# Optimization experiments

Measured on AMD Instinct MI355X. Metric: run time of the kernel, lower is better.

Reference implementation:

```python
import jax, jax.numpy as jnp
import numpy as np

MUL0, MUL1, SCALARS_OUT = 16, 16, 128
L0, L1 = MUL0, MUL1 * 3            # 16, 48
PATH_NUMEL = MUL0 * MUL1 * SCALARS_OUT  # 32768 per path, two paths
EPS = 1e-5
# e3nn normalization: irrep_normalization='component' -> alpha = dim(ir_out) = 1;
# path_normalization='element' -> divide by sum over paths to same output of mul1*mul2 = 256+256 = 512.
PATH_COEFF = 1.0 / np.sqrt(512.0)
CG_110 = 1.0 / np.sqrt(3.0)  # wigner_3j(1,1,0)[i,j] = delta_ij/sqrt(3) (unit Frobenius norm)


def layer_norm(x, g, b):
    mu = jnp.mean(x, axis=-1, keepdims=True)
    var = jnp.mean(jnp.square(x - mu), axis=-1, keepdims=True)
    return (x - mu) * jax.lax.rsqrt(var + EPS) * g + b


def ff_block(x, g, b, w1, w2, b2):
    # LayerNorm -> Linear(no bias) -> SiLU -> Linear(bias); residual=False in both uses
    h = jax.nn.silu(layer_norm(x, g, b) @ w1)
    return h @ w2 + b2


def setup_inputs() -> dict:
    key = jax.random.key(0)
    ks = jax.random.split(key, 8)
    N = 2048
    return {
        "x": jax.random.normal(ks[0], (N, L0 + L1), dtype=jnp.float32),
        "we_ln_g": jnp.ones((L0,), jnp.float32),
        "we_ln_b": jnp.zeros((L0,), jnp.float32),
        "we_w1": jax.random.normal(ks[1], (L0, 4 * L0), jnp.float32) / np.sqrt(L0),
        "we_w2": jax.random.normal(ks[2], (4 * L0, 2 * PATH_NUMEL), jnp.float32) / np.sqrt(4 * L0),
        "we_b2": jnp.zeros((2 * PATH_NUMEL,), jnp.float32),
        "om_ln_g": jnp.ones((SCALARS_OUT,), jnp.float32),
        "om_ln_b": jnp.zeros((SCALARS_OUT,), jnp.float32),
        "om_w1": jax.random.normal(ks[3], (SCALARS_OUT, 4 * SCALARS_OUT), jnp.float32) / np.sqrt(SCALARS_OUT),
        "om_w2": jax.random.normal(ks[4], (4 * SCALARS_OUT, 1), jnp.float32) / np.sqrt(4 * SCALARS_OUT),
        "om_b2": jnp.zeros((1,), jnp.float32),
    }


def reference(x, we_ln_g, we_ln_b, we_w1, we_w2, we_b2,
              om_ln_g, om_ln_b, om_w1, om_w2, om_b2):
    N = x.shape[0]
    feats = x[:, :L0]                       # [N, 16] scalars (0e)
    x1 = x[:, L0:].reshape(N, MUL1, 3)      # [N, 16, 3] vectors (1o)

    # per-sample tensor-product weights (shared_weights=False)
    w = ff_block(feats, we_ln_g, we_ln_b, we_w1, we_w2, we_b2)  # [N, 65536]
    w0 = w[:, :PATH_NUMEL].reshape(N, MUL0, MUL0, SCALARS_OUT)
    w1 = w[:, PATH_NUMEL:].reshape(N, MUL1, MUL1, SCALARS_OUT)

    # path 0: 0e x 0e -> 0e  (uvw)
    o0 = jnp.einsum('nu,nv,nuvw->nw', feats, feats, w0)
    # path 1: 1o x 1o -> 0e  (uvw, CG = delta_ij/sqrt(3))
    o1 = jnp.einsum('nui,nvi,nuvw->nw', x1, x1, w1) * CG_110
    tp_out = PATH_COEFF * (o0 + o1)          # [N, 128]

    return ff_block(tp_out, om_ln_g, om_ln_b, om_w1, om_w2, om_b2)  # [N, 1]
```

## Files before the change

kernel.cpp:

```cpp
#include <hip/hip_runtime.h>
#include <hip/hip_bf16.h>
#include <cstdint>

#define EPS 1e-5f
#define PATH_COEFF 0.04419417382415922f
#define CG110     0.5773502691896258f

typedef __bf16 v8bf __attribute__((ext_vector_type(8)));
typedef float  v4f  __attribute__((ext_vector_type(4)));
typedef _Float16 v4h __attribute__((ext_vector_type(4)));

static __device__ __forceinline__ unsigned short f2bf(float x){
    unsigned int u = __builtin_bit_cast(unsigned int, x);
    u += 0x7fffu + ((u >> 16) & 1u);
    return (unsigned short)(u >> 16);
}
static __device__ __forceinline__ unsigned short f2h(float x){
    return __builtin_bit_cast(unsigned short, (_Float16)x);
}

__global__ __launch_bounds__(256)
void k_pre(const float* __restrict__ w2, const float* __restrict__ b2,
           unsigned short* __restrict__ Vt2,
           const float* __restrict__ om_w1, unsigned short* __restrict__ w1t,
           const float* __restrict__ x, const float* __restrict__ lng,
           const float* __restrict__ lnb, const float* __restrict__ we_w1,
           unsigned short* __restrict__ Q2, float* __restrict__ Ht, int N)
{
    __shared__ __align__(16) unsigned short tile[32][128];
    __shared__ __align__(16) uint4 qtile[64][4];
    __shared__ float htile[4][65];
    int b = blockIdx.x;
    int t = threadIdx.x;

    if (b < 260){
        int k    = b >> 2;
        int slab = b & 3;
        const float* srcbase = (k < 64) ? (w2 + (size_t)k * 65536) : b2;
        for (int chunk = 0; chunk < 4; ++chunk){
            int pbase = slab*128 + chunk*32;
            #pragma unroll
            for (int i = 0; i < 4; ++i){
                int g = t + 256*i;
                int ploc = g >> 5, c4 = g & 31;
                const float4 v = *(const float4*)(srcbase + (size_t)(pbase + ploc)*128 + c4*4);
                unsigned int w0 = (unsigned)f2bf(v.x) | ((unsigned)f2bf(v.y) << 16);
                unsigned int w1 = (unsigned)f2bf(v.z) | ((unsigned)f2bf(v.w) << 16);
                *(uint2*)&tile[ploc][c4*4] = make_uint2(w0, w1);
            }
            __syncthreads();
            int w = t & 127, h = t >> 7;
            int ps = slab*4 + chunk;
            unsigned int words[8];
            #pragma unroll
            for (int g2 = 0; g2 < 8; ++g2)
                words[g2] = (unsigned)tile[h*16 + g2*2][w] | ((unsigned)tile[h*16 + g2*2 + 1][w] << 16);
            unsigned short* dq0 = Vt2 + (((size_t)(k*16 + ps)*4 + 2*h    )*128 + w)*8;
            unsigned short* dq1 = Vt2 + (((size_t)(k*16 + ps)*4 + 2*h + 1)*128 + w)*8;
            *(uint4*)dq0 = make_uint4(words[0], words[1], words[2], words[3]);
            *(uint4*)dq1 = make_uint4(words[4], words[5], words[6], words[7]);
            __syncthreads();
        }
    } else if (b < 264){
        int j0 = (b - 260) * 128;
        for (int chunk = 0; chunk < 4; ++chunk){
            #pragma unroll
            for (int i = 0; i < 4; ++i){
                int g = t + 256*i;
                int wloc = g >> 5, c4 = g & 31;
                int w = chunk*32 + wloc;
                const float4 v = *(const float4*)(om_w1 + (size_t)w*512 + j0 + c4*4);
                unsigned int a = (unsigned)f2bf(v.x) | ((unsigned)f2bf(v.y) << 16);
                unsigned int bb = (unsigned)f2bf(v.z) | ((unsigned)f2bf(v.w) << 16);
                *(uint2*)&tile[wloc][c4*4] = make_uint2(a, bb);
            }
            __syncthreads();
            int jl = t & 127, h = t >> 7;
            unsigned int words[8];
            #pragma unroll
            for (int g2 = 0; g2 < 8; ++g2)
                words[g2] = (unsigned)tile[h*16 + g2*2][jl] | ((unsigned)tile[h*16 + g2*2 + 1][jl] << 16);
            unsigned short* dst = w1t + (size_t)(j0 + jl)*128 + chunk*32 + h*16;
            *(uint4*)dst       = make_uint4(words[0], words[1], words[2], words[3]);
            *(uint4*)(dst + 8) = make_uint4(words[4], words[5], words[6], words[7]);
            __syncthreads();
        }
    } else {
        int wv = t >> 6, lane = t & 63;
        int row0 = (b - 264)*4;
        int row  = row0 + wv;
        const float* xr = x + (size_t)row * 64;
        float f[16]; float mu = 0.f;
        #pragma unroll
        for (int u = 0; u < 16; ++u){ f[u] = xr[u]; mu += f[u]; }
        mu *= (1.f/16.f);
        float var = 0.f;
        #pragma unroll
        for (int u = 0; u < 16; ++u){ float d = f[u] - mu; var += d*d; }
        var *= (1.f/16.f);
        float inv = rsqrtf(var + EPS);
        float lnf[16];
        #pragma unroll
        for (int u = 0; u < 16; ++u) lnf[u] = (f[u]-mu)*inv*lng[u] + lnb[u];
        float h1 = 0.f;
        #pragma unroll
        for (int u = 0; u < 16; ++u) h1 += lnf[u] * we_w1[u*64 + lane];
        float h = h1 / (1.f + expf(-h1));
        htile[wv][lane] = h;
        if (lane == 0) htile[wv][64] = 1.f;

        union { unsigned short qs[8]; uint4 v; } qu;
        #pragma unroll
        for (int j = 0; j < 8; ++j){
            int p = lane*8 + j;
            float q;
            if (p < 256){
                int u = p >> 4, v = p & 15;
                q = PATH_COEFF * f[u] * f[v];
            } else {
                int pp = p - 256;
                int u = pp >> 4, v = pp & 15;
                const float* ya = xr + 16 + u*3;
                const float* yb = xr + 16 + v*3;
                q = (PATH_COEFF * CG110) * (ya[0]*yb[0] + ya[1]*yb[1] + ya[2]*yb[2]);
            }
            qu.qs[j] = f2bf(q);
        }
        qtile[lane][wv] = qu.v;
        __syncthreads();

        int rb = row0 >> 6, r64base = row0 & 63;
        {
            int slot = t >> 2, rr = t & 3;
            ((uint4*)Q2)[(size_t)rb*4096 + (size_t)slot*64 + r64base + rr] = qtile[slot][rr];
        }
        if (t < 65){
            float4 hv = make_float4(htile[0][t], htile[1][t], htile[2][t], htile[3][t]);
            *(float4*)(Ht + (size_t)t*N + row0) = hv;
        }
    }
}

__global__ __launch_bounds__(256, 2)
void k_main(const unsigned short* __restrict__ Q2, const unsigned short* __restrict__ Vt2,
            const float* __restrict__ Ht, unsigned short* __restrict__ partial, int N)
{
    __shared__ __align__(16) unsigned short stile[4][64*72];
    int g = blockIdx.x & 7;
    int j = blockIdx.x >> 3;
    int kg, mb;
    if (j < 64){ mb = j >> 2; kg = g*4 + (j & 3); }
    else { if (g != 0) return; mb = j - 64; kg = 32; }

    int tid  = threadIdx.x;
    int lane = tid & 63, wv = tid >> 6;
    int r2 = wv >> 1, c2 = wv & 1;
    int quad = lane >> 4, l16 = lane & 15;
    int rowbase = mb*128 + r2*64;
    int rb = rowbase >> 6;
    int wbase = c2*64;

    int k0 = kg*2;
    int k1 = (kg == 32) ? 64 : k0 + 1;
    float sel = (kg == 32) ? 0.f : 1.f;

    const unsigned short* aroot  = Q2  + (size_t)rb*32768 + quad*512  + l16*8;
    const unsigned short* broot0 = Vt2 + (size_t)k0*65536 + quad*1024 + (wbase + l16)*8;
    const unsigned short* broot1 = Vt2 + (size_t)k1*65536 + quad*1024 + (wbase + l16)*8;

    v4f accA[4][4], accB[4][4];
    #pragma unroll
    for (int m=0;m<4;++m)
      #pragma unroll
      for (int n=0;n<4;++n)
        #pragma unroll
        for (int r=0;r<4;++r){ accA[m][n][r] = 0.f; accB[m][n][r] = 0.f; }

    #pragma unroll 2
    for (int ps = 0; ps < 16; ++ps){
        const unsigned short* ap  = aroot  + ps*2048;
        const unsigned short* bp0 = broot0 + ps*4096;
        const unsigned short* bp1 = broot1 + ps*4096;
        v8bf a[4], b0[4], b1[4];
        #pragma unroll
        for (int m=0;m<4;++m) a[m]  = *(const v8bf*)(ap  + m*128);
        #pragma unroll
        for (int n=0;n<4;++n) b0[n] = *(const v8bf*)(bp0 + n*128);
        #pragma unroll
        for (int n=0;n<4;++n) b1[n] = *(const v8bf*)(bp1 + n*128);
        #pragma unroll
        for (int m=0;m<4;++m)
          #pragma unroll
          for (int n=0;n<4;++n)
            accA[m][n] = __builtin_amdgcn_mfma_f32_16x16x32_bf16(a[m], b0[n], accA[m][n], 0, 0, 0);
        #pragma unroll
        for (int m=0;m<4;++m)
          #pragma unroll
          for (int n=0;n<4;++n)
            accB[m][n] = __builtin_amdgcn_mfma_f32_16x16x32_bf16(a[m], b1[n], accB[m][n], 0, 0, 0);
    }

    const float* hp0 = Ht + (size_t)k0*N + rowbase + quad*4;
    const float* hp1 = Ht + (size_t)k1*N + rowbase + quad*4;
    unsigned short* my = stile[wv];
    #pragma unroll
    for (int m=0;m<4;++m){
        v4f h0 = *(const v4f*)(hp0 + m*16);
        v4f h1 = *(const v4f*)(hp1 + m*16);
        #pragma unroll
        for (int n=0;n<4;++n)
          #pragma unroll
          for (int r=0;r<4;++r)
            my[(m*16 + quad*4 + r)*72 + n*16 + l16] =
                f2h(h0[r]*accA[m][n][r] + sel*h1[r]*accB[m][n][r]);
    }
    unsigned short* gp = partial + ((size_t)(mb*33 + kg))*16384
                                 + (size_t)(r2*64)*128 + wbase;
    #pragma unroll
    for (int i = 0; i < 8; ++i){
        int row = i*8 + (lane >> 3);
        int c16 = (lane & 7)*8;
        uint4 v = *(const uint4*)&my[row*72 + c16];
        *(uint4*)(gp + (size_t)row*128 + c16) = v;
    }
}

__global__ __launch_bounds__(128)
void k_tail(const unsigned short* __restrict__ partial, const float* __restrict__ g,
            const float* __restrict__ b, const unsigned short* __restrict__ w1t,
            const float* __restrict__ w2, const float* __restrict__ b2,
            float* __restrict__ out, int N)
{
    __shared__ __align__(16) unsigned short lnf_lds[16][128];
    __shared__ float red2[2][16];
    int t = threadIdx.x;
    int rowbase = blockIdx.x * 16;
    int mb = rowbase >> 7;
    const unsigned short* pbase = partial + (size_t)mb*33*16384;

    #pragma unroll
    for (int half = 0; half < 2; ++half){
        int rl  = half*8 + (t >> 4);
        int w8  = (t & 15) * 8;
        int row = rowbase + rl;
        int rin = row & 127;
        const unsigned short* p0 = pbase + (size_t)rin*128 + w8;

        float s[8];
        #pragma unroll
        for (int j2 = 0; j2 < 8; ++j2) s[j2] = 0.f;
        #pragma unroll 11
        for (int sl = 0; sl < 33; ++sl){
            uint4 raw = *(const uint4*)(p0 + (size_t)sl*16384);
            union { uint4 u; _Float16 h[8]; } cv; cv.u = raw;
            #pragma unroll
            for (int j2 = 0; j2 < 8; ++j2) s[j2] += (float)cv.h[j2];
        }
        float sum = 0.f, sq = 0.f;
        #pragma unroll
        for (int j2 = 0; j2 < 8; ++j2){ sum += s[j2]; sq += s[j2]*s[j2]; }
        #pragma unroll
        for (int off = 8; off > 0; off >>= 1){
            sum += __shfl_xor(sum, off, 16);
            sq  += __shfl_xor(sq,  off, 16);
        }
        float mu  = sum * (1.f/128.f);
        float var = sq * (1.f/128.f) - mu*mu;
        float inv = rsqrtf(var + EPS);
        unsigned short o[8];
        #pragma unroll
        for (int j2 = 0; j2 < 8; ++j2)
            o[j2] = f2bf((s[j2]-mu)*inv*g[w8+j2] + b[w8+j2]);
        *(uint4*)&lnf_lds[rl][w8] = *(uint4*)o;
    }
    __syncthreads();

    int lane = t & 63, wv = t >> 6;
    int quad = lane >> 4, l16 = lane & 15;
    int jbase = wv * 256;

    v4f acc[16];
    #pragma unroll
    for (int n=0;n<16;++n)
      #pragma unroll
      for (int r=0;r<4;++r) acc[n][r] = 0.f;

    #pragma unroll
    for (int ps = 0; ps < 4; ++ps){
        v8bf a = *(const v8bf*)&lnf_lds[l16][ps*32 + quad*8];
        v8bf bb[16];
        #pragma unroll
        for (int n=0;n<16;++n)
            bb[n] = *(const v8bf*)(w1t + (size_t)(jbase + n*16 + l16)*128 + ps*32 + quad*8);
        #pragma unroll
        for (int n=0;n<16;++n)
            acc[n] = __builtin_amdgcn_mfma_f32_16x16x32_bf16(a, bb[n], acc[n], 0, 0, 0);
    }

    float w2v[16];
    #pragma unroll
    for (int n=0;n<16;++n) w2v[n] = w2[jbase + n*16 + l16];

    #pragma unroll
    for (int r=0;r<4;++r){
        float s = 0.f;
        #pragma unroll
        for (int n=0;n<16;++n){
            float v = acc[n][r];
            s += (v / (1.f + expf(-v))) * w2v[n];
        }
        #pragma unroll
        for (int off=8; off>0; off>>=1) s += __shfl_xor(s, off, 16);
        if (l16 == 0) red2[wv][quad*4 + r] = s;
    }
    __syncthreads();
    if (t < 16)
        out[rowbase + t] = red2[0][t] + red2[1][t] + b2[0];
}

extern "C" void kernel_launch(void* const* d_in, const int* in_sizes, int n_in,
                              void* d_out, int out_size, void* d_ws, size_t ws_size,
                              hipStream_t stream)
{
    const float* x     = (const float*)d_in[0];
    const float* we_g  = (const float*)d_in[1];
    const float* we_b  = (const float*)d_in[2];
    const float* we_w1 = (const float*)d_in[3];
    const float* we_w2 = (const float*)d_in[4];
    const float* we_b2 = (const float*)d_in[5];
    const float* om_g  = (const float*)d_in[6];
    const float* om_b  = (const float*)d_in[7];
    const float* om_w1 = (const float*)d_in[8];
    const float* om_w2 = (const float*)d_in[9];
    const float* om_b2 = (const float*)d_in[10];

    int N  = in_sizes[0] / 64;

    char* ws = (char*)d_ws;
    size_t offV = 0;
    size_t szV  = (size_t)65*16*4*128*8*2;
    size_t offQ = offV + szV;
    size_t szQ  = (size_t)N*512*2;
    size_t offH = offQ + szQ;
    size_t szH  = (size_t)65*N*4;
    size_t offP = offH + szH;
    size_t szP  = (size_t)(N/128)*33*16384*2;
    size_t offL = offP + szP;
    size_t szL  = (size_t)N*128*2;
    size_t offW = offL + szL;

    unsigned short* Vt2 = (unsigned short*)(ws + offV);
    unsigned short* Q2  = (unsigned short*)(ws + offQ);
    float* Ht           = (float*)(ws + offH);
    unsigned short* Par = (unsigned short*)(ws + offP);
    unsigned short* W1t = (unsigned short*)(ws + offW);
    float* out = (float*)d_out;

    hipLaunchKernelGGL(k_pre,  dim3(264 + N/4), dim3(256), 0, stream,
                       we_w2, we_b2, Vt2, om_w1, W1t, x, we_g, we_b, we_w1, Q2, Ht, N);
    hipLaunchKernelGGL(k_main, dim3(80*8),      dim3(256), 0, stream, Q2, Vt2, Ht, Par, N);
    hipLaunchKernelGGL(k_tail, dim3(N/16),      dim3(128), 0, stream,
                       Par, om_g, om_b, W1t, om_w2, om_b2, out, N);
}
```

Before: 135.0 us.

## Double-buffer k_main operands in LDS via global_load_lds and widen k_tail

k_main now stages its A and B MFMA operands through a double-buffered LDS tile using direct global-to-LDS loads, so each tile is fetched once per block and the next stage's fetch overlaps the current MFMAs. This removes redundant global/L2 reads across waves that share the same operands. The cost is one block-wide barrier per k-step and more LDS per block, which can reduce occupancy. Separately, k_tail runs with 256 threads, so each thread handles one row slice and each wave covers 128 hidden columns instead of 256, lowering per-thread work and register use.

```diff
diff --git a/kernel.cpp b/kernel.cpp
--- a/kernel.cpp
+++ b/kernel.cpp
@@ -17,6 +17,11 @@
 }
 static __device__ __forceinline__ unsigned short f2h(float x){
     return __builtin_bit_cast(unsigned short, (_Float16)x);
+}
+static __device__ __forceinline__ void gload16(const unsigned short* g, unsigned short* l){
+    __builtin_amdgcn_global_load_lds(
+        (const __attribute__((address_space(1))) unsigned int*)g,
+        (__attribute__((address_space(3))) unsigned int*)l, 16, 0, 0);
 }
 
 __global__ __launch_bounds__(256)
@@ -145,7 +150,7 @@
 void k_main(const unsigned short* __restrict__ Q2, const unsigned short* __restrict__ Vt2,
             const float* __restrict__ Ht, unsigned short* __restrict__ partial, int N)
 {
-    __shared__ __align__(16) unsigned short stile[4][64*72];
+    __shared__ __align__(16) unsigned short sbuf[2][12288];
     int g = blockIdx.x & 7;
     int j = blockIdx.x >> 3;
     int kg, mb;
@@ -157,16 +162,32 @@
     int r2 = wv >> 1, c2 = wv & 1;
     int quad = lane >> 4, l16 = lane & 15;
     int rowbase = mb*128 + r2*64;
-    int rb = rowbase >> 6;
+    int rb0 = (mb*128) >> 6;
     int wbase = c2*64;
 
     int k0 = kg*2;
     int k1 = (kg == 32) ? 64 : k0 + 1;
     float sel = (kg == 32) ? 0.f : 1.f;
 
-    const unsigned short* aroot  = Q2  + (size_t)rb*32768 + quad*512  + l16*8;
-    const unsigned short* broot0 = Vt2 + (size_t)k0*65536 + quad*1024 + (wbase + l16)*8;
-    const unsigned short* broot1 = Vt2 + (size_t)k1*65536 + quad*1024 + (wbase + l16)*8;
+    const unsigned short* gA0 = Q2  + (size_t)rb0*32768;
+    const unsigned short* gA1 = Q2  + (size_t)(rb0+1)*32768;
+    const unsigned short* gB0 = Vt2 + (size_t)k0*65536;
+    const unsigned short* gB1 = Vt2 + (size_t)k1*65536;
+
+#define STAGE(BUF, PS)                                                        \
+    {                                                                         \
+        unsigned short* lb_ = &sbuf[BUF][0];                                  \
+        _Pragma("unroll")                                                     \
+        for (int c_ = 0; c_ < 6; ++c_){                                       \
+            int j_ = wv + c_*4;                                               \
+            const unsigned short* gs_;                                        \
+            if (j_ < 4)       gs_ = gA0 + (PS)*2048 + j_*512;                 \
+            else if (j_ < 8)  gs_ = gA1 + (PS)*2048 + (j_-4)*512;             \
+            else if (j_ < 16) gs_ = gB0 + (PS)*4096 + (j_-8)*512;             \
+            else              gs_ = gB1 + (PS)*4096 + (j_-16)*512;            \
+            gload16(gs_ + lane*8, lb_ + j_*512 + lane*8);                     \
+        }                                                                     \
+    }
 
     v4f accA[4][4], accB[4][4];
     #pragma unroll
@@ -176,18 +197,23 @@
         #pragma unroll
         for (int r=0;r<4;++r){ accA[m][n][r] = 0.f; accB[m][n][r] = 0.f; }
 
-    #pragma unroll 2
+    STAGE(0, 0);
+    __syncthreads();
+
+    int abase = r2*2048 + quad*512 + l16*8;
+    int bbase = quad*1024 + wbase*8 + l16*8;
+
+    int buf = 0;
     for (int ps = 0; ps < 16; ++ps){
-        const unsigned short* ap  = aroot  + ps*2048;
-        const unsigned short* bp0 = broot0 + ps*4096;
-        const unsigned short* bp1 = broot1 + ps*4096;
+        if (ps < 15) STAGE(buf^1, ps+1);
+        const unsigned short* lbuf = &sbuf[buf][0];
         v8bf a[4], b0[4], b1[4];
         #pragma unroll
-        for (int m=0;m<4;++m) a[m]  = *(const v8bf*)(ap  + m*128);
-        #pragma unroll
-        for (int n=0;n<4;++n) b0[n] = *(const v8bf*)(bp0 + n*128);
-        #pragma unroll
-        for (int n=0;n<4;++n) b1[n] = *(const v8bf*)(bp1 + n*128);
+        for (int m=0;m<4;++m) a[m]  = *(const v8bf*)(lbuf + abase + m*128);
+        #pragma unroll
+        for (int n=0;n<4;++n) b0[n] = *(const v8bf*)(lbuf + 4096 + bbase + n*128);
+        #pragma unroll
+        for (int n=0;n<4;++n) b1[n] = *(const v8bf*)(lbuf + 8192 + bbase + n*128);
         #pragma unroll
         for (int m=0;m<4;++m)
           #pragma unroll
@@ -198,11 +224,14 @@
           #pragma unroll
           for (int n=0;n<4;++n)
             accB[m][n] = __builtin_amdgcn_mfma_f32_16x16x32_bf16(a[m], b1[n], accB[m][n], 0, 0, 0);
-    }
+        __syncthreads();
+        buf ^= 1;
+    }
+#undef STAGE
 
     const float* hp0 = Ht + (size_t)k0*N + rowbase + quad*4;
     const float* hp1 = Ht + (size_t)k1*N + rowbase + quad*4;
-    unsigned short* my = stile[wv];
+    unsigned short* my = &sbuf[0][0] + wv*4608;
     #pragma unroll
     for (int m=0;m<4;++m){
         v4f h0 = *(const v4f*)(hp0 + m*16);
@@ -225,25 +254,23 @@
     }
 }
 
-__global__ __launch_bounds__(128)
+__global__ __launch_bounds__(256)
 void k_tail(const unsigned short* __restrict__ partial, const float* __restrict__ g,
             const float* __restrict__ b, const unsigned short* __restrict__ w1t,
             const float* __restrict__ w2, const float* __restrict__ b2,
             float* __restrict__ out, int N)
 {
     __shared__ __align__(16) unsigned short lnf_lds[16][128];
-    __shared__ float red2[2][16];
+    __shared__ float red2[4][16];
     int t = threadIdx.x;
     int rowbase = blockIdx.x * 16;
     int mb = rowbase >> 7;
     const unsigned short* pbase = partial + (size_t)mb*33*16384;
 
-    #pragma unroll
-    for (int half = 0; half < 2; ++half){
-        int rl  = half*8 + (t >> 4);
+    {
+        int rl  = t >> 4;
         int w8  = (t & 15) * 8;
-        int row = rowbase + rl;
-        int rin = row & 127;
+        int rin = (rowbase + rl) & 127;
         const unsigned short* p0 = pbase + (size_t)rin*128 + w8;
 
         float s[8];
@@ -277,35 +304,35 @@
 
     int lane = t & 63, wv = t >> 6;
     int quad = lane >> 4, l16 = lane & 15;
-    int jbase = wv * 256;
-
-    v4f acc[16];
-    #pragma unroll
-    for (int n=0;n<16;++n)
+    int jbase = wv * 128;
+
+    v4f acc[8];
+    #pragma unroll
+    for (int n=0;n<8;++n)
       #pragma unroll
       for (int r=0;r<4;++r) acc[n][r] = 0.f;
 
     #pragma unroll
     for (int ps = 0; ps < 4; ++ps){
         v8bf a = *(const v8bf*)&lnf_lds[l16][ps*32 + quad*8];
-        v8bf bb[16];
-        #pragma unroll
-        for (int n=0;n<16;++n)
+        v8bf bb[8];
+        #pragma unroll
+        for (int n=0;n<8;++n)
             bb[n] = *(const v8bf*)(w1t + (size_t)(jbase + n*16 + l16)*128 + ps*32 + quad*8);
         #pragma unroll
-        for (int n=0;n<16;++n)
+        for (int n=0;n<8;++n)
             acc[n] = __builtin_amdgcn_mfma_f32_16x16x32_bf16(a, bb[n], acc[n], 0, 0, 0);
     }
 
-    float w2v[16];
-    #pragma unroll
-    for (int n=0;n<16;++n) w2v[n] = w2[jbase + n*16 + l16];
+    float w2v[8];
+    #pragma unroll
+    for (int n=0;n<8;++n) w2v[n] = w2[jbase + n*16 + l16];
 
     #pragma unroll
     for (int r=0;r<4;++r){
         float s = 0.f;
         #pragma unroll
-        for (int n=0;n<16;++n){
+        for (int n=0;n<8;++n){
             float v = acc[n][r];
             s += (v / (1.f + expf(-v))) * w2v[n];
         }
@@ -315,7 +342,7 @@
     }
     __syncthreads();
     if (t < 16)
-        out[rowbase + t] = red2[0][t] + red2[1][t] + b2[0];
+        out[rowbase + t] = red2[0][t] + red2[1][t] + red2[2][t] + red2[3][t] + b2[0];
 }
 
 extern "C" void kernel_launch(void* const* d_in, const int* in_sizes, int n_in,
@@ -359,6 +386,6 @@
     hipLaunchKernelGGL(k_pre,  dim3(264 + N/4), dim3(256), 0, stream,
                        we_w2, we_b2, Vt2, om_w1, W1t, x, we_g, we_b, we_w1, Q2, Ht, N);
     hipLaunchKernelGGL(k_main, dim3(80*8),      dim3(256), 0, stream, Q2, Vt2, Ht, Par, N);
-    hipLaunchKernelGGL(k_tail, dim3(N/16),      dim3(128), 0, stream,
+    hipLaunchKernelGGL(k_tail, dim3(N/16),      dim3(256), 0, stream,
                        Par, om_g, om_b, W1t, om_w2, om_b2, out, N);
 }
```

Result: faster. 126.8 us (-6.1%).
